# Kernel optimization log

Measured on AMD Instinct MI355X. Metric: run time of the kernel, lower is better.

Reference implementation:

```python
import jax, jax.numpy as jnp
import numpy as np

B, N, M, D, H = 8, 2048, 2048, 512, 8


def setup_inputs() -> dict:
    key = jax.random.key(0)
    ks = jax.random.split(key, 12)
    std = D ** (-0.5)
    inp = {
        "k": jax.random.normal(ks[0], (B, N, D), jnp.float32),
        "v": jax.random.normal(ks[1], (B, N, D), jnp.float32),
        "q": jax.random.normal(ks[2], (B, M, D), jnp.float32),
        # per-head projections, stacked over the head axis: [H, D, D]
        "Wk": jax.random.normal(ks[3], (H, D, D), jnp.float32) * std,
        "bk": jax.random.normal(ks[4], (H, D), jnp.float32) * 0.01,
        "Wv": jax.random.normal(ks[5], (H, D, D), jnp.float32) * std,
        "bv": jax.random.normal(ks[6], (H, D), jnp.float32) * 0.01,
        "Wq": jax.random.normal(ks[7], (H, D, D), jnp.float32) * std,
        "bq": jax.random.normal(ks[8], (H, D), jnp.float32) * 0.01,
        # final linear: input ordering is (hidden_dim, head) flattened -> H*D
        "Wo": jax.random.normal(ks[9], (H * D, D), jnp.float32) * (H * D) ** (-0.5),
        "bo": jax.random.normal(ks[10], (D,), jnp.float32) * 0.01,
    }
    return inp


def reference(k, v, q, Wk, bk, Wv, bv, Wq, bq, Wo, bo):
    # Per-head linear projections (torch loops over heads; here batched over h).
    # nn.Linear computes x @ W.T + b; Wk here stores W.T directly as [H, D, D].
    k_ = jnp.einsum("bnd,hde->bhne", k, Wk) + bk[None, :, None, :]  # [B,H,N,D]
    v_ = jnp.einsum("bnd,hde->bhne", v, Wv) + bv[None, :, None, :]  # [B,H,N,D]
    q_ = jnp.einsum("bmd,hde->bhme", q, Wq) + bq[None, :, None, :]  # [B,H,M,D]

    scale = D ** 0.5
    scores = jnp.einsum("bhmd,bhnd->bhmn", q_, k_) / scale  # [B,H,M,N]
    weights = jax.nn.softmax(scores, axis=-1)
    out = jnp.einsum("bhmn,bhnd->bhmd", weights, v_)  # [B,H,M,D]

    # torch: stack(outs, dim=-1) -> [B,M,D,H], then view -> [B,M,D*H]
    outs = jnp.transpose(out, (0, 2, 3, 1)).reshape(B, M, D * H)
    # matching flatten order (d-major, h-minor) requires Wo rows ordered d*H+h;
    # setup generates Wo random so any consistent ordering is faithful.
    rep = outs @ Wo + bo  # [B,M,D]
    return rep
```

## Files before the change

kernel.cpp:

```cpp
#include <hip/hip_runtime.h>
#include <hip/hip_bf16.h>
#include <cstdint>
#include <cstddef>

typedef __bf16 bf16x8 __attribute__((ext_vector_type(8)));
typedef __bf16 bf16x4 __attribute__((ext_vector_type(4)));
typedef float floatx4 __attribute__((ext_vector_type(4)));

#define MFMA16(a, b, c) __builtin_amdgcn_mfma_f32_16x16x32_bf16((a), (b), (c), 0, 0, 0)

__device__ __forceinline__ void load_lds16(const __bf16* g, __bf16* l) {
  __builtin_amdgcn_global_load_lds(
      (const __attribute__((address_space(1))) uint32_t*)(g),
      (__attribute__((address_space(3))) uint32_t*)(l), 16, 0, 0);
}

#define BAR_LGKM()                                        \
  do {                                                    \
    asm volatile("s_waitcnt lgkmcnt(0)" ::: "memory");    \
    __builtin_amdgcn_s_barrier();                         \
    __builtin_amdgcn_sched_barrier(0);                    \
  } while (0)

__global__ __launch_bounds__(256) void tw_t(const float* __restrict__ W,
                                            __bf16* __restrict__ Wt, float scale) {
  __shared__ float tile[64][65];
  int h = blockIdx.z, d0 = blockIdx.y * 64, e0 = blockIdx.x * 64;
  int tx = threadIdx.x & 15, ty = threadIdx.x >> 4;
  const float* src = W + ((size_t)h * 512 + d0) * 512 + e0;
#pragma unroll
  for (int j = 0; j < 4; ++j) {
    int dd = ty + j * 16;
    float4 f = *(const float4*)&src[(size_t)dd * 512 + tx * 4];
    tile[dd][tx * 4 + 0] = f.x; tile[dd][tx * 4 + 1] = f.y;
    tile[dd][tx * 4 + 2] = f.z; tile[dd][tx * 4 + 3] = f.w;
  }
  __syncthreads();
  __bf16* dst = Wt + ((size_t)h * 512 + e0) * 512 + d0;
#pragma unroll
  for (int j = 0; j < 4; ++j) {
    int ee = ty + j * 16;
    bf16x4 v;
#pragma unroll
    for (int x = 0; x < 4; ++x) v[x] = (__bf16)(tile[tx * 4 + x][ee] * scale);
    *(bf16x4*)&dst[(size_t)ee * 512 + tx * 4] = v;
  }
}

__global__ __launch_bounds__(256) void wo_t(const float* __restrict__ Wo,
                                            __bf16* __restrict__ Wot) {
  __shared__ float tile[64][65];
  int h = blockIdx.z, d0 = blockIdx.y * 64, e0 = blockIdx.x * 64;
  int tx = threadIdx.x & 15, ty = threadIdx.x >> 4;
#pragma unroll
  for (int j = 0; j < 4; ++j) {
    int dd = ty + j * 16;
    float4 f = *(const float4*)&Wo[(size_t)((d0 + dd) * 8 + h) * 512 + e0 + tx * 4];
    tile[dd][tx * 4 + 0] = f.x; tile[dd][tx * 4 + 1] = f.y;
    tile[dd][tx * 4 + 2] = f.z; tile[dd][tx * 4 + 3] = f.w;
  }
  __syncthreads();
#pragma unroll
  for (int j = 0; j < 4; ++j) {
    int ee = ty + j * 16;
    bf16x4 v;
#pragma unroll
    for (int x = 0; x < 4; ++x) v[x] = (__bf16)tile[tx * 4 + x][ee];
    *(bf16x4*)&Wot[(size_t)(e0 + ee) * 4096 + h * 512 + d0 + tx * 4] = v;
  }
}

__global__ __launch_bounds__(256) void cvt_bf16(const float* __restrict__ in,
                                                __bf16* __restrict__ out, int n8) {
  int i = blockIdx.x * 256 + threadIdx.x;
  if (i < n8) {
    float4 f0 = *(const float4*)&in[(size_t)i * 8];
    float4 f1 = *(const float4*)&in[(size_t)i * 8 + 4];
    bf16x8 v;
    v[0] = (__bf16)f0.x; v[1] = (__bf16)f0.y; v[2] = (__bf16)f0.z; v[3] = (__bf16)f0.w;
    v[4] = (__bf16)f1.x; v[5] = (__bf16)f1.y; v[6] = (__bf16)f1.z; v[7] = (__bf16)f1.w;
    *(bf16x8*)&out[(size_t)i * 8] = v;
  }
}

template <int EPI, bool AF32>
__global__ __launch_bounds__(256) void gemm_bt(const void* __restrict__ Ap,
                                               const __bf16* __restrict__ Bt,
                                               const float* __restrict__ bias,
                                               void* __restrict__ Cout,
                                               int N, int K, float bscale) {
  __shared__ __align__(16) __bf16 sA[128][72];
  __shared__ __align__(16) __bf16 sB[128][72];
  const int tid = threadIdx.x;
  const int lane = tid & 63;
  const int wave = tid >> 6;
  const int lr = lane & 15;
  const int lq = lane >> 4;
  const int wm = (wave >> 1) * 64;
  const int wn = (wave & 1) * 64;
  const int bx = blockIdx.x, by = blockIdx.y;
  const int srow = tid >> 3;
  const int scol = (tid & 7) << 3;

  const floatx4 z4 = {0.f, 0.f, 0.f, 0.f};
  floatx4 acc[4][4];
#pragma unroll
  for (int i = 0; i < 4; ++i)
#pragma unroll
    for (int j = 0; j < 4; ++j) acc[i][j] = z4;

  const size_t abase = (size_t)(by * 128) * K;
  const size_t bbase = (size_t)(bx * 128) * K;

  for (int k0 = 0; k0 < K; k0 += 64) {
#pragma unroll
    for (int p = 0; p < 4; ++p) {
      int row = p * 32 + srow;
      if (AF32) {
        const float* A = (const float*)Ap;
        float4 f0 = *(const float4*)&A[abase + (size_t)row * K + k0 + scol];
        float4 f1 = *(const float4*)&A[abase + (size_t)row * K + k0 + scol + 4];
        bf16x8 v;
        v[0] = (__bf16)f0.x; v[1] = (__bf16)f0.y; v[2] = (__bf16)f0.z; v[3] = (__bf16)f0.w;
        v[4] = (__bf16)f1.x; v[5] = (__bf16)f1.y; v[6] = (__bf16)f1.z; v[7] = (__bf16)f1.w;
        *(bf16x8*)&sA[row][scol] = v;
      } else {
        const __bf16* A = (const __bf16*)Ap;
        *(bf16x8*)&sA[row][scol] = *(const bf16x8*)&A[abase + (size_t)row * K + k0 + scol];
      }
      *(bf16x8*)&sB[row][scol] = *(const bf16x8*)&Bt[bbase + (size_t)row * K + k0 + scol];
    }
    __syncthreads();
#pragma unroll
    for (int ks = 0; ks < 2; ++ks) {
      bf16x8 af[4], bfr[4];
#pragma unroll
      for (int mt = 0; mt < 4; ++mt)
        af[mt] = *(const bf16x8*)&sA[wm + mt * 16 + lr][ks * 32 + lq * 8];
#pragma unroll
      for (int nt = 0; nt < 4; ++nt)
        bfr[nt] = *(const bf16x8*)&sB[wn + nt * 16 + lr][ks * 32 + lq * 8];
#pragma unroll
      for (int mt = 0; mt < 4; ++mt)
#pragma unroll
        for (int nt = 0; nt < 4; ++nt) acc[mt][nt] = MFMA16(af[mt], bfr[nt], acc[mt][nt]);
    }
    __syncthreads();
  }

#pragma unroll
  for (int mt = 0; mt < 4; ++mt) {
#pragma unroll
    for (int nt = 0; nt < 4; ++nt) {
      int col = bx * 128 + wn + nt * 16 + lr;
      int row0 = by * 128 + wm + mt * 16 + lq * 4;
      float bcol = bias[col] * bscale;
      if (EPI == 0) {
        __bf16* dst = (__bf16*)Cout;
        int h = col >> 9, e = col & 511;
#pragma unroll
        for (int r = 0; r < 4; ++r) {
          int row = row0 + r;
          int b = row >> 11, m = row & 2047;
          dst[((size_t)((b << 3) | h) * 2048 + m) * 512 + e] = (__bf16)(acc[mt][nt][r] + bcol);
        }
      } else if (EPI == 1) {
        __bf16* dst = (__bf16*)Cout;
        int h = col >> 9, e = col & 511;
        int b = row0 >> 11, n = row0 & 2047;
        bf16x4 pk;
#pragma unroll
        for (int r = 0; r < 4; ++r) pk[r] = (__bf16)(acc[mt][nt][r] + bcol);
        *(bf16x4*)&dst[((size_t)((b << 3) | h) * 512 + e) * 2048 + n] = pk;
      } else {
        float* dst = (float*)Cout;
#pragma unroll
        for (int r = 0; r < 4; ++r) {
          int row = row0 + r;
          dst[(size_t)row * N + col] = acc[mt][nt][r] + bcol;
        }
      }
    }
  }
}

__global__ __launch_bounds__(512, 2) void attn_kernel(const __bf16* __restrict__ Qp,
                                                      const __bf16* __restrict__ Kp,
                                                      const __bf16* __restrict__ Vt,
                                                      __bf16* __restrict__ Outs) {
  __shared__ __align__(16) __bf16 kls[2][32 * 512];
  __shared__ __align__(16) __bf16 vls[2][512 * 32];
  __shared__ __align__(16) __bf16 pls[128 * 40];
  __shared__ __align__(16) floatx4 sx[2][8][64];
  __shared__ __align__(16) float l_red[128];
  const int tid = threadIdx.x;
  const int lane = tid & 63;
  const int wave = tid >> 6;
  const int lr = lane & 15;
  const int lq = lane >> 4;
  const int blk = blockIdx.x;
  const int bh = blk >> 4;
  const int mblk = blk & 15;
  const int rp = (wave & 3) * 2;
  const int dh = wave >> 2;
  const int fg = rp + dh;
  const int e0 = wave * 64;
  const int mbase = mblk * 128;
  const __bf16* Qb = Qp + (size_t)bh * (2048 * 512);
  const __bf16* Kb = Kp + (size_t)bh * (2048 * 512);
  const __bf16* Vb = Vt + (size_t)bh * (512 * 2048);

  int gK[4], gV[4];
#pragma unroll
  for (int i = 0; i < 4; ++i) {
    int q = i * 512 + tid;
    int rK = q >> 6;
    gK[i] = rK * 512 + ((q & 63) ^ (rK & 7)) * 8;
    int eV = q >> 2;
    gV[i] = eV * 2048 + ((q & 3) ^ (eV & 3)) * 8;
  }

  bf16x8 qf[2][8];
#pragma unroll
  for (int ks = 0; ks < 8; ++ks) {
    qf[0][ks] = *(const bf16x8*)&Qb[(size_t)(mbase + fg * 16 + lr) * 512 +
                                    dh * 256 + ks * 32 + lq * 8];
    qf[1][ks] = *(const bf16x8*)&Qb[(size_t)(mbase + (rp + (dh ^ 1)) * 16 + lr) * 512 +
                                    dh * 256 + ks * 32 + lq * 8];
  }

  const floatx4 z4 = {0.f, 0.f, 0.f, 0.f};
  floatx4 o[8][4];
#pragma unroll
  for (int mt = 0; mt < 8; ++mt)
#pragma unroll
    for (int et = 0; et < 4; ++et) o[mt][et] = z4;
  float lsum[4] = {0.f, 0.f, 0.f, 0.f};

#pragma unroll
  for (int i = 0; i < 4; ++i) {
    load_lds16(Kb + gK[i], &kls[0][i * 4096 + wave * 512]);
    load_lds16(Vb + gV[i], &vls[0][i * 4096 + wave * 512]);
  }
  __syncthreads();

  for (int t = 0; t < 64; ++t) {
    const int cur = t & 1;
    if (t < 63) {
      const __bf16* kg = Kb + (size_t)(t + 1) * (32 * 512);
      const __bf16* vg = Vb + (t + 1) * 32;
#pragma unroll
      for (int i = 0; i < 4; ++i) {
        load_lds16(kg + gK[i], &kls[cur ^ 1][i * 4096 + wave * 512]);
        load_lds16(vg + gV[i], &vls[cur ^ 1][i * 4096 + wave * 512]);
      }
    }
    floatx4 sm0 = z4, sm1 = z4, sp0 = z4, sp1 = z4;
    const __bf16* kc = kls[cur];
#pragma unroll
    for (int ks = 0; ks < 8; ++ks) {
      int cidx = ((dh * 32 + ks * 4 + lq) ^ (lr & 7)) * 8;
      bf16x8 k0 = *(const bf16x8*)&kc[lr * 512 + cidx];
      bf16x8 k1 = *(const bf16x8*)&kc[(16 + lr) * 512 + cidx];
      sm0 = MFMA16(qf[0][ks], k0, sm0);
      sm1 = MFMA16(qf[0][ks], k1, sm1);
      sp0 = MFMA16(qf[1][ks], k0, sp0);
      sp1 = MFMA16(qf[1][ks], k1, sp1);
    }
    sx[0][wave][lane] = sp0;
    sx[1][wave][lane] = sp1;
    BAR_LGKM();
    {
      floatx4 q0 = sx[0][wave ^ 4][lane];
      floatx4 q1 = sx[1][wave ^ 4][lane];
#pragma unroll
      for (int r = 0; r < 4; ++r) {
        float p0 = __expf(sm0[r] + q0[r]);
        float p1 = __expf(sm1[r] + q1[r]);
        lsum[r] += p0 + p1;
        pls[(fg * 16 + lq * 4 + r) * 40 + lr] = (__bf16)p0;
        pls[(fg * 16 + lq * 4 + r) * 40 + 16 + lr] = (__bf16)p1;
      }
    }
    BAR_LGKM();
    {
      const __bf16* vc = vls[cur];
      bf16x8 vf[4];
#pragma unroll
      for (int et = 0; et < 4; ++et) {
        int e = e0 + et * 16 + lr;
        vf[et] = *(const bf16x8*)&vc[e * 32 + ((lq ^ (e & 3)) * 8)];
      }
#pragma unroll
      for (int mt = 0; mt < 8; ++mt) {
        bf16x8 pf = *(const bf16x8*)&pls[(mt * 16 + lr) * 40 + lq * 8];
#pragma unroll
        for (int et = 0; et < 4; ++et) o[mt][et] = MFMA16(pf, vf[et], o[mt][et]);
      }
    }
    __syncthreads();
  }

#pragma unroll
  for (int r = 0; r < 4; ++r) {
    float s = lsum[r];
    s += __shfl_xor(s, 1);
    s += __shfl_xor(s, 2);
    s += __shfl_xor(s, 4);
    s += __shfl_xor(s, 8);
    lsum[r] = s;
  }
  if (lr == 0) {
#pragma unroll
    for (int r = 0; r < 4; ++r) l_red[fg * 16 + lq * 4 + r] = lsum[r];
  }
  __syncthreads();

  int b = bh >> 3, h = bh & 7;
#pragma unroll
  for (int mt = 0; mt < 8; ++mt) {
    float4 lv = *(const float4*)&l_red[mt * 16 + lq * 4];
    float invr[4] = {1.0f / lv.x, 1.0f / lv.y, 1.0f / lv.z, 1.0f / lv.w};
    size_t rowbase = ((size_t)b * 2048 + mbase + mt * 16 + lq * 4) * 4096 + h * 512 + e0;
#pragma unroll
    for (int et = 0; et < 4; ++et)
#pragma unroll
      for (int r = 0; r < 4; ++r)
        Outs[rowbase + (size_t)r * 4096 + et * 16 + lr] = (__bf16)(o[mt][et][r] * invr[r]);
  }
}

extern "C" void kernel_launch(void* const* d_in, const int* in_sizes, int n_in,
                              void* d_out, int out_size, void* d_ws, size_t ws_size,
                              hipStream_t stream) {
  (void)in_sizes; (void)n_in; (void)out_size;
  const float* kin = (const float*)d_in[0];
  const float* vin = (const float*)d_in[1];
  const float* qin = (const float*)d_in[2];
  const float* Wk  = (const float*)d_in[3];
  const float* bk  = (const float*)d_in[4];
  const float* Wv  = (const float*)d_in[5];
  const float* bv  = (const float*)d_in[6];
  const float* Wq  = (const float*)d_in[7];
  const float* bq  = (const float*)d_in[8];
  const float* Wo  = (const float*)d_in[9];
  const float* bo  = (const float*)d_in[10];
  float* out = (float*)d_out;
  char* ws = (char*)d_ws;

  const float scale = 0.044194173824159216f;

  const size_t SZ_W = (size_t)4096 * 512 * 2;
  const size_t SZ_B = (size_t)8 * 2048 * 512 * 2;
  const size_t FIXED = 4 * SZ_W;

  int nb = 1;
  if (ws_size >= FIXED + 8 * 4 * SZ_B) nb = 8;
  else if (ws_size >= FIXED + 4 * 4 * SZ_B) nb = 4;
  else if (ws_size >= FIXED + 2 * 4 * SZ_B) nb = 2;

  __bf16* Wkt = (__bf16*)(ws);
  __bf16* Wvt = (__bf16*)(ws + SZ_W);
  __bf16* Wqt = (__bf16*)(ws + 2 * SZ_W);
  __bf16* Wot = (__bf16*)(ws + 3 * SZ_W);
  char* chunkbase = ws + FIXED;
  __bf16* kproj = (__bf16*)(chunkbase);
  __bf16* qproj = (__bf16*)(chunkbase + (size_t)nb * SZ_B);
  __bf16* vt    = (__bf16*)(chunkbase + (size_t)nb * 2 * SZ_B);
  __bf16* outs  = (__bf16*)(chunkbase + (size_t)nb * 3 * SZ_B);

  tw_t<<<dim3(8, 8, 8), dim3(256), 0, stream>>>(Wk, Wkt, 1.0f);
  tw_t<<<dim3(8, 8, 8), dim3(256), 0, stream>>>(Wv, Wvt, 1.0f);
  tw_t<<<dim3(8, 8, 8), dim3(256), 0, stream>>>(Wq, Wqt, scale);
  wo_t<<<dim3(8, 8, 8), dim3(256), 0, stream>>>(Wo, Wot);

  for (int b0 = 0; b0 < 8; b0 += nb) {
    const float* kc = kin + (size_t)b0 * 2048 * 512;
    const float* vc = vin + (size_t)b0 * 2048 * 512;
    const float* qc = qin + (size_t)b0 * 2048 * 512;
    const size_t chunk_els = (size_t)nb * 2048 * 512;
    __bf16* kb16 = outs;
    __bf16* qb16 = outs + chunk_els;
    __bf16* vb16 = outs + 2 * chunk_els;
    int n8 = (int)(chunk_els / 8);
    int cvgrid = (n8 + 255) / 256;
    cvt_bf16<<<dim3(cvgrid), dim3(256), 0, stream>>>(kc, kb16, n8);
    cvt_bf16<<<dim3(cvgrid), dim3(256), 0, stream>>>(qc, qb16, n8);
    cvt_bf16<<<dim3(cvgrid), dim3(256), 0, stream>>>(vc, vb16, n8);
    gemm_bt<0, false><<<dim3(32, nb * 16), dim3(256), 0, stream>>>((void*)kb16, Wkt, bk, (void*)kproj, 4096, 512, 1.0f);
    gemm_bt<0, false><<<dim3(32, nb * 16), dim3(256), 0, stream>>>((void*)qb16, Wqt, bq, (void*)qproj, 4096, 512, scale);
    gemm_bt<1, false><<<dim3(32, nb * 16), dim3(256), 0, stream>>>((void*)vb16, Wvt, bv, (void*)vt, 4096, 512, 1.0f);
    attn_kernel<<<dim3(nb * 128), dim3(512), 0, stream>>>(qproj, kproj, vt, outs);
    gemm_bt<2, false><<<dim3(4, nb * 16), dim3(256), 0, stream>>>(
        (void*)outs, Wot, bo, (void*)(out + (size_t)b0 * 2048 * 512), 512, 4096, 1.0f);
  }
}
```

Measured before the change: 1.540 ms.

## Use direct global-to-LDS loads in GEMM, XCD block swizzle and MFMA priority in attention

The projection GEMMs now stage A and B tiles with global_load_lds DMA into unpadded LDS instead of register round-trips, and the unused fp32 A path is dropped. The attention kernel remaps block ids so blocks sharing a batch-head land on the same XCD for L2 reuse. It also raises wave priority around the MFMA loops with s_setprio. Removing the LDS padding may introduce bank conflicts on the fragment reads.

```diff
diff --git a/kernel.cpp b/kernel.cpp
--- a/kernel.cpp
+++ b/kernel.cpp
@@ -21,6 +21,12 @@
     __builtin_amdgcn_s_barrier();                         \
     __builtin_amdgcn_sched_barrier(0);                    \
   } while (0)
+
+__device__ __forceinline__ int xcd_swizzle(int orig, int nwg) {
+  int q = nwg >> 3, r = nwg & 7;
+  int xcd = orig & 7, local = orig >> 3;
+  return (xcd < r) ? xcd * (q + 1) + local : r * (q + 1) + (xcd - r) * q + local;
+}
 
 __global__ __launch_bounds__(256) void tw_t(const float* __restrict__ W,
                                             __bf16* __restrict__ Wt, float scale) {
@@ -83,14 +89,14 @@
   }
 }
 
-template <int EPI, bool AF32>
-__global__ __launch_bounds__(256) void gemm_bt(const void* __restrict__ Ap,
+template <int EPI>
+__global__ __launch_bounds__(256) void gemm_bt(const __bf16* __restrict__ A,
                                                const __bf16* __restrict__ Bt,
                                                const float* __restrict__ bias,
                                                void* __restrict__ Cout,
                                                int N, int K, float bscale) {
-  __shared__ __align__(16) __bf16 sA[128][72];
-  __shared__ __align__(16) __bf16 sB[128][72];
+  __shared__ __align__(16) __bf16 sA[128 * 64];
+  __shared__ __align__(16) __bf16 sB[128 * 64];
   const int tid = threadIdx.x;
   const int lane = tid & 63;
   const int wave = tid >> 6;
@@ -99,8 +105,6 @@
   const int wm = (wave >> 1) * 64;
   const int wn = (wave & 1) * 64;
   const int bx = blockIdx.x, by = blockIdx.y;
-  const int srow = tid >> 3;
-  const int scol = (tid & 7) << 3;
 
   const floatx4 z4 = {0.f, 0.f, 0.f, 0.f};
   floatx4 acc[4][4];
@@ -111,24 +115,14 @@
 
   const size_t abase = (size_t)(by * 128) * K;
   const size_t bbase = (size_t)(bx * 128) * K;
+  const int col8 = (tid & 7) << 3;
 
   for (int k0 = 0; k0 < K; k0 += 64) {
 #pragma unroll
     for (int p = 0; p < 4; ++p) {
-      int row = p * 32 + srow;
-      if (AF32) {
-        const float* A = (const float*)Ap;
-        float4 f0 = *(const float4*)&A[abase + (size_t)row * K + k0 + scol];
-        float4 f1 = *(const float4*)&A[abase + (size_t)row * K + k0 + scol + 4];
-        bf16x8 v;
-        v[0] = (__bf16)f0.x; v[1] = (__bf16)f0.y; v[2] = (__bf16)f0.z; v[3] = (__bf16)f0.w;
-        v[4] = (__bf16)f1.x; v[5] = (__bf16)f1.y; v[6] = (__bf16)f1.z; v[7] = (__bf16)f1.w;
-        *(bf16x8*)&sA[row][scol] = v;
-      } else {
-        const __bf16* A = (const __bf16*)Ap;
-        *(bf16x8*)&sA[row][scol] = *(const bf16x8*)&A[abase + (size_t)row * K + k0 + scol];
-      }
-      *(bf16x8*)&sB[row][scol] = *(const bf16x8*)&Bt[bbase + (size_t)row * K + k0 + scol];
+      int row = (p * 256 + tid) >> 3;
+      load_lds16(&A[abase + (size_t)row * K + k0 + col8], &sA[p * 2048 + wave * 512]);
+      load_lds16(&Bt[bbase + (size_t)row * K + k0 + col8], &sB[p * 2048 + wave * 512]);
     }
     __syncthreads();
 #pragma unroll
@@ -136,10 +130,10 @@
       bf16x8 af[4], bfr[4];
 #pragma unroll
       for (int mt = 0; mt < 4; ++mt)
-        af[mt] = *(const bf16x8*)&sA[wm + mt * 16 + lr][ks * 32 + lq * 8];
+        af[mt] = *(const bf16x8*)&sA[(wm + mt * 16 + lr) * 64 + ks * 32 + lq * 8];
 #pragma unroll
       for (int nt = 0; nt < 4; ++nt)
-        bfr[nt] = *(const bf16x8*)&sB[wn + nt * 16 + lr][ks * 32 + lq * 8];
+        bfr[nt] = *(const bf16x8*)&sB[(wn + nt * 16 + lr) * 64 + ks * 32 + lq * 8];
 #pragma unroll
       for (int mt = 0; mt < 4; ++mt)
 #pragma unroll
@@ -198,7 +192,7 @@
   const int wave = tid >> 6;
   const int lr = lane & 15;
   const int lq = lane >> 4;
-  const int blk = blockIdx.x;
+  const int blk = xcd_swizzle(blockIdx.x, gridDim.x);
   const int bh = blk >> 4;
   const int mblk = blk & 15;
   const int rp = (wave & 3) * 2;
@@ -257,6 +251,7 @@
     }
     floatx4 sm0 = z4, sm1 = z4, sp0 = z4, sp1 = z4;
     const __bf16* kc = kls[cur];
+    __builtin_amdgcn_s_setprio(1);
 #pragma unroll
     for (int ks = 0; ks < 8; ++ks) {
       int cidx = ((dh * 32 + ks * 4 + lq) ^ (lr & 7)) * 8;
@@ -267,6 +262,7 @@
       sp0 = MFMA16(qf[1][ks], k0, sp0);
       sp1 = MFMA16(qf[1][ks], k1, sp1);
     }
+    __builtin_amdgcn_s_setprio(0);
     sx[0][wave][lane] = sp0;
     sx[1][wave][lane] = sp1;
     BAR_LGKM();
@@ -291,12 +287,14 @@
         int e = e0 + et * 16 + lr;
         vf[et] = *(const bf16x8*)&vc[e * 32 + ((lq ^ (e & 3)) * 8)];
       }
+      __builtin_amdgcn_s_setprio(1);
 #pragma unroll
       for (int mt = 0; mt < 8; ++mt) {
         bf16x8 pf = *(const bf16x8*)&pls[(mt * 16 + lr) * 40 + lq * 8];
 #pragma unroll
         for (int et = 0; et < 4; ++et) o[mt][et] = MFMA16(pf, vf[et], o[mt][et]);
       }
+      __builtin_amdgcn_s_setprio(0);
     }
     __syncthreads();
   }
@@ -387,11 +385,11 @@
     cvt_bf16<<<dim3(cvgrid), dim3(256), 0, stream>>>(kc, kb16, n8);
     cvt_bf16<<<dim3(cvgrid), dim3(256), 0, stream>>>(qc, qb16, n8);
     cvt_bf16<<<dim3(cvgrid), dim3(256), 0, stream>>>(vc, vb16, n8);
-    gemm_bt<0, false><<<dim3(32, nb * 16), dim3(256), 0, stream>>>((void*)kb16, Wkt, bk, (void*)kproj, 4096, 512, 1.0f);
-    gemm_bt<0, false><<<dim3(32, nb * 16), dim3(256), 0, stream>>>((void*)qb16, Wqt, bq, (void*)qproj, 4096, 512, scale);
-    gemm_bt<1, false><<<dim3(32, nb * 16), dim3(256), 0, stream>>>((void*)vb16, Wvt, bv, (void*)vt, 4096, 512, 1.0f);
+    gemm_bt<0><<<dim3(32, nb * 16), dim3(256), 0, stream>>>(kb16, Wkt, bk, (void*)kproj, 4096, 512, 1.0f);
+    gemm_bt<0><<<dim3(32, nb * 16), dim3(256), 0, stream>>>(qb16, Wqt, bq, (void*)qproj, 4096, 512, scale);
+    gemm_bt<1><<<dim3(32, nb * 16), dim3(256), 0, stream>>>(vb16, Wvt, bv, (void*)vt, 4096, 512, 1.0f);
     attn_kernel<<<dim3(nb * 128), dim3(512), 0, stream>>>(qproj, kproj, vt, outs);
-    gemm_bt<2, false><<<dim3(4, nb * 16), dim3(256), 0, stream>>>(
-        (void*)outs, Wot, bo, (void*)(out + (size_t)b0 * 2048 * 512), 512, 4096, 1.0f);
-  }
-}
+    gemm_bt<2><<<dim3(4, nb * 16), dim3(256), 0, stream>>>(
+        outs, Wot, bo, (void*)(out + (size_t)b0 * 2048 * 512), 512, 4096, 1.0f);
+  }
+}
```

New measurement: 1.645 ms. 1.07x slower.
